# Kernel optimization log

Measured on AMD Instinct MI355X. Metric: run time of the kernel, lower is better.

Reference implementation:

```python
import jax, jax.numpy as jnp
import numpy as np

B, IN, HID, LAT, EH = 32768, 512, 2048, 128, 512
MID = max(HID // 2, LAT * 2)      # 1024
HALF = max(EH // 2, 4)            # 256
EPS = 1e-5
LN10 = float(np.log(10.0))


def setup_inputs() -> dict:
    key = jax.random.key(0)
    ks = jax.random.split(key, 24)
    r = lambda k, shp, s=0.02: (jax.random.normal(k, shp, dtype=jnp.float32) * s)
    d = {
        "x": jax.random.normal(ks[0], (B, IN), dtype=jnp.float32),
        "group_idx": jax.random.randint(ks[1], (B,), 0, 3),
        # encoder: Linear(IN,HID)+BN+ELU, Linear(HID,MID)+BN+ELU, Linear(MID,LAT)
        "e_w1": r(ks[2], (HID, IN)), "e_b1": jnp.zeros((HID,), jnp.float32),
        "e_g1": jnp.ones((HID,), jnp.float32), "e_be1": jnp.zeros((HID,), jnp.float32),
        "e_w2": r(ks[3], (MID, HID)), "e_b2": jnp.zeros((MID,), jnp.float32),
        "e_g2": jnp.ones((MID,), jnp.float32), "e_be2": jnp.zeros((MID,), jnp.float32),
        "e_w3": r(ks[4], (LAT, MID)), "e_b3": jnp.zeros((LAT,), jnp.float32),
        # shared: Linear(LAT+IN,HID)+BN+ELU, Linear(HID,MID)+BN+ELU
        "s_w1": r(ks[5], (HID, LAT + IN)), "s_b1": jnp.zeros((HID,), jnp.float32),
        "s_g1": jnp.ones((HID,), jnp.float32), "s_be1": jnp.zeros((HID,), jnp.float32),
        "s_w2": r(ks[6], (MID, HID)), "s_b2": jnp.zeros((MID,), jnp.float32),
        "s_g2": jnp.ones((MID,), jnp.float32), "s_be2": jnp.zeros((MID,), jnp.float32),
        # 3 expert heads, stacked on leading axis E=3
        "h_w1": r(ks[7], (3, EH, MID)), "h_b1": jnp.zeros((3, EH), jnp.float32),
        "h_w2": r(ks[8], (3, HALF, EH)), "h_b2": jnp.zeros((3, HALF), jnp.float32),
        "h_w3": r(ks[9], (3, HALF)), "h_b3": jnp.zeros((3,), jnp.float32),
    }
    return d


def _bn(h, g, b):
    # BatchNorm1d in training mode: batch mean, biased batch var
    m = jnp.mean(h, axis=0)
    v = jnp.var(h, axis=0)
    return (h - m) * (g / jnp.sqrt(v + EPS)) + b


def _elu(h):
    return jax.nn.elu(h)


def reference(x, group_idx,
              e_w1, e_b1, e_g1, e_be1, e_w2, e_b2, e_g2, e_be2, e_w3, e_b3,
              s_w1, s_b1, s_g1, s_be1, s_w2, s_b2, s_g2, s_be2,
              h_w1, h_b1, h_w2, h_b2, h_w3, h_b3):
    # encoder
    h = _elu(_bn(x @ e_w1.T + e_b1, e_g1, e_be1))
    h = _elu(_bn(h @ e_w2.T + e_b2, e_g2, e_be2))
    latent = h @ e_w3.T + e_b3                              # [B, LAT]
    # shared trunk
    z = jnp.concatenate([latent, x], axis=-1)               # [B, LAT+IN]
    h = _elu(_bn(z @ s_w1.T + s_b1, s_g1, s_be1))
    hidden = _elu(_bn(h @ s_w2.T + s_b2, s_g2, s_be2))      # [B, MID]
    # expert heads: compute all 3 (tiny vs trunk), then select per-row group
    t1 = _elu(jnp.einsum('bm,ehm->ebh', hidden, h_w1) + h_b1[:, None, :])   # [3,B,EH]
    t2 = _elu(jnp.einsum('ebh,efh->ebf', t1, h_w2) + h_b2[:, None, :])      # [3,B,HALF]
    pred_all = jnp.einsum('ebf,ef->eb', t2, h_w3) + h_b3[:, None]           # [3,B]
    pred_raw = jnp.take_along_axis(pred_all, group_idx[None, :], axis=0)[0] # [B]
    pred_log = -jax.nn.softplus(pred_raw)
    pred_prob = jnp.exp(pred_log * jnp.float32(LN10))       # 10 ** pred_log
    return pred_log, pred_prob
```

## Files before the change

### kernel.cpp

```cpp
#include <hip/hip_runtime.h>
#include <math.h>

#define B_    32768
#define LN10_ 2.302585092994046f
#define MT_H  264
#define NBLK  128

typedef __attribute__((ext_vector_type(8))) short short8;
typedef __attribute__((ext_vector_type(4))) float f32x4;

typedef const __attribute__((address_space(1))) void gvoid_t;
typedef __attribute__((address_space(3))) void svoid_t;

__device__ __forceinline__ void gl16(const void* g, void* l) {
  __builtin_amdgcn_global_load_lds((gvoid_t*)g, (svoid_t*)l, 16, 0, 0);
}

__device__ __forceinline__ float bf2f(unsigned int u) {
  union { unsigned int i; float f; } v; v.i = u << 16; return v.f;
}
__device__ __forceinline__ unsigned short f2bf(float f) {
  union { float f; unsigned int i; } v; v.f = f;
  unsigned int x = v.i;
  unsigned int r = x + 0x7FFFu + ((x >> 16) & 1u);
  return (unsigned short)(r >> 16);
}

__global__ __launch_bounds__(512)
void gemm256(const unsigned short* __restrict__ A0_, int lda,
             const unsigned short* __restrict__ W0_, int ldw,
             unsigned short* __restrict__ C0, int ldc, int K,
             float* __restrict__ st, int Ntot) {
  __shared__ __align__(16) unsigned short lds[65536];
  const int t = threadIdx.x;
  const int nx = gridDim.x, ny = gridDim.y;
  const int f = blockIdx.y * nx + blockIdx.x;
  const int xcd = f & 7, g = f >> 3;
  const int gdiv = g / nx;
  const int mt = xcd * (ny >> 3) + gdiv;
  const int nt = g - gdiv * nx;
  const int mBase = mt * 256, nBase = nt * 256;
  const unsigned short* Ap = A0_ + (size_t)mBase * lda;
  const unsigned short* Wp = W0_ + (size_t)nBase * ldw;
  const int w = t >> 6, l = t & 63;
  const int wr = w >> 2, wc = w & 3;
  const int lm = l & 15, lg = l >> 4;

  const int rr = t >> 3;
  const int xc = ((t & 7) ^ (rr & 7)) << 3;
  const unsigned short* gA = Ap + (size_t)rr * lda + xc;
  const unsigned short* gB = Wp + (size_t)rr * ldw + xc;

#define SG(ptr, ld, rowoff, dst) \
    gl16((ptr) + (size_t)(rowoff) * (ld) + ko_, &lds[(dst) + t * 8])
#define STAGE_Aa(tt) { const int d_=((tt)&1)<<15; const size_t ko_=(size_t)(tt)*64; \
    SG(gA,lda,0,d_);          SG(gA,lda,128,d_+8192); }
#define STAGE_Ab(tt) { const int d_=((tt)&1)<<15; const size_t ko_=(size_t)(tt)*64; \
    SG(gA,lda,64,d_+4096);    SG(gA,lda,192,d_+12288); }
#define STAGE_B0(tt) { const int d_=((tt)&1)<<15; const size_t ko_=(size_t)(tt)*64; \
    SG(gB,ldw,0,d_+16384);    SG(gB,ldw,64,d_+20480); }
#define STAGE_B1(tt) { const int d_=((tt)&1)<<15; const size_t ko_=(size_t)(tt)*64; \
    SG(gB,ldw,128,d_+24576);  SG(gB,ldw,192,d_+28672); }

  const int cs0 = ((lg) ^ (l & 7)) << 3;
  const int cs1 = ((4 | lg) ^ (l & 7)) << 3;

  f32x4 acc[8][4];
#pragma unroll
  for (int i = 0; i < 8; ++i)
#pragma unroll
    for (int j = 0; j < 4; ++j) {
      f32x4 z4 = {0.f, 0.f, 0.f, 0.f};
      acc[i][j] = z4;
    }

  const int NT = K >> 6;
  STAGE_Aa(0); STAGE_B0(0); STAGE_B1(0); STAGE_Ab(0);
  if (NT > 1) {
    STAGE_Aa(1); STAGE_B0(1); STAGE_B1(1);
    asm volatile("s_waitcnt vmcnt(6)" ::: "memory");
  } else {
    asm volatile("s_waitcnt vmcnt(0)" ::: "memory");
  }
  __builtin_amdgcn_s_barrier();
  __builtin_amdgcn_sched_barrier(0);

  short8 af[4][2], b01[2][2], b23[2][2];
  for (int tt = 0; tt < NT; ++tt) {
    const int d = (tt & 1) << 15;
    const int abase = d + (wr * 128 + lm) * 64;
    const int bbase = d + 16384 + (wc * 32 + lm) * 64;
    const bool s1ok = (tt + 1 < NT), s2ok = (tt + 2 < NT);
#pragma unroll
    for (int fi = 0; fi < 4; ++fi) {
      af[fi][0] = *(const short8*)&lds[abase + fi * 1024 + cs0];
      af[fi][1] = *(const short8*)&lds[abase + fi * 1024 + cs1];
    }
#pragma unroll
    for (int fj = 0; fj < 2; ++fj) {
      b01[fj][0] = *(const short8*)&lds[bbase + fj * 1024 + cs0];
      b01[fj][1] = *(const short8*)&lds[bbase + fj * 1024 + cs1];
    }
    if (s1ok) STAGE_Ab(tt + 1);
    __builtin_amdgcn_s_barrier();
    asm volatile("s_waitcnt lgkmcnt(0)" ::: "memory");
    __builtin_amdgcn_sched_barrier(0);
    __builtin_amdgcn_s_setprio(1);
#pragma unroll
    for (int fi = 0; fi < 4; ++fi) {
      acc[fi][0] = __builtin_amdgcn_mfma_f32_16x16x32_bf16(af[fi][0], b01[0][0], acc[fi][0], 0, 0, 0);
      acc[fi][0] = __builtin_amdgcn_mfma_f32_16x16x32_bf16(af[fi][1], b01[0][1], acc[fi][0], 0, 0, 0);
      acc[fi][1] = __builtin_amdgcn_mfma_f32_16x16x32_bf16(af[fi][0], b01[1][0], acc[fi][1], 0, 0, 0);
      acc[fi][1] = __builtin_amdgcn_mfma_f32_16x16x32_bf16(af[fi][1], b01[1][1], acc[fi][1], 0, 0, 0);
    }
    __builtin_amdgcn_s_setprio(0);
#pragma unroll
    for (int fj = 0; fj < 2; ++fj) {
      b23[fj][0] = *(const short8*)&lds[bbase + 8192 + fj * 1024 + cs0];
      b23[fj][1] = *(const short8*)&lds[bbase + 8192 + fj * 1024 + cs1];
    }
    if (s2ok) STAGE_Aa(tt + 2);
    __builtin_amdgcn_s_barrier();
    asm volatile("s_waitcnt lgkmcnt(0)" ::: "memory");
    __builtin_amdgcn_sched_barrier(0);
    __builtin_amdgcn_s_setprio(1);
#pragma unroll
    for (int fi = 0; fi < 4; ++fi) {
      acc[fi][2] = __builtin_amdgcn_mfma_f32_16x16x32_bf16(af[fi][0], b23[0][0], acc[fi][2], 0, 0, 0);
      acc[fi][2] = __builtin_amdgcn_mfma_f32_16x16x32_bf16(af[fi][1], b23[0][1], acc[fi][2], 0, 0, 0);
      acc[fi][3] = __builtin_amdgcn_mfma_f32_16x16x32_bf16(af[fi][0], b23[1][0], acc[fi][3], 0, 0, 0);
      acc[fi][3] = __builtin_amdgcn_mfma_f32_16x16x32_bf16(af[fi][1], b23[1][1], acc[fi][3], 0, 0, 0);
    }
    __builtin_amdgcn_s_setprio(0);
#pragma unroll
    for (int fi = 0; fi < 4; ++fi) {
      af[fi][0] = *(const short8*)&lds[abase + 4096 + fi * 1024 + cs0];
      af[fi][1] = *(const short8*)&lds[abase + 4096 + fi * 1024 + cs1];
    }
    if (s2ok) STAGE_B0(tt + 2);
    __builtin_amdgcn_s_barrier();
    asm volatile("s_waitcnt lgkmcnt(0)" ::: "memory");
    __builtin_amdgcn_sched_barrier(0);
    __builtin_amdgcn_s_setprio(1);
#pragma unroll
    for (int fi = 0; fi < 4; ++fi) {
      acc[4 + fi][0] = __builtin_amdgcn_mfma_f32_16x16x32_bf16(af[fi][0], b01[0][0], acc[4 + fi][0], 0, 0, 0);
      acc[4 + fi][0] = __builtin_amdgcn_mfma_f32_16x16x32_bf16(af[fi][1], b01[0][1], acc[4 + fi][0], 0, 0, 0);
      acc[4 + fi][1] = __builtin_amdgcn_mfma_f32_16x16x32_bf16(af[fi][0], b01[1][0], acc[4 + fi][1], 0, 0, 0);
      acc[4 + fi][1] = __builtin_amdgcn_mfma_f32_16x16x32_bf16(af[fi][1], b01[1][1], acc[4 + fi][1], 0, 0, 0);
    }
    __builtin_amdgcn_s_setprio(0);
    if (s2ok) STAGE_B1(tt + 2);
    __builtin_amdgcn_s_setprio(1);
#pragma unroll
    for (int fi = 0; fi < 4; ++fi) {
      acc[4 + fi][2] = __builtin_amdgcn_mfma_f32_16x16x32_bf16(af[fi][0], b23[0][0], acc[4 + fi][2], 0, 0, 0);
      acc[4 + fi][2] = __builtin_amdgcn_mfma_f32_16x16x32_bf16(af[fi][1], b23[0][1], acc[4 + fi][2], 0, 0, 0);
      acc[4 + fi][3] = __builtin_amdgcn_mfma_f32_16x16x32_bf16(af[fi][0], b23[1][0], acc[4 + fi][3], 0, 0, 0);
      acc[4 + fi][3] = __builtin_amdgcn_mfma_f32_16x16x32_bf16(af[fi][1], b23[1][1], acc[4 + fi][3], 0, 0, 0);
    }
    __builtin_amdgcn_s_setprio(0);
    if (s1ok) {
      if (s2ok) { asm volatile("s_waitcnt vmcnt(6)" ::: "memory"); }
      else      { asm volatile("s_waitcnt vmcnt(0)" ::: "memory"); }
      __builtin_amdgcn_s_barrier();
      __builtin_amdgcn_sched_barrier(0);
    }
  }

#pragma unroll
  for (int j = 0; j < 4; ++j) {
    int n = nBase + (j >> 1) * 128 + wc * 32 + (j & 1) * 16 + lm;
    float s1 = 0.f, q1 = 0.f;
#pragma unroll
    for (int i = 0; i < 8; ++i) {
      int m0 = mBase + wr * 128 + i * 16 + lg * 4;
#pragma unroll
      for (int r = 0; r < 4; ++r) {
        float v = acc[i][j][r];
        s1 += v; q1 += v * v;
        C0[(size_t)(m0 + r) * ldc + n] = f2bf(v);
      }
    }
    s1 += __shfl_xor(s1, 16, 64); s1 += __shfl_xor(s1, 32, 64);
    q1 += __shfl_xor(q1, 16, 64); q1 += __shfl_xor(q1, 32, 64);
    if (lg == 0) { atomicAdd(&st[n], s1); atomicAdd(&st[Ntot + n], q1); }
  }
}
#undef SG
#undef STAGE_Aa
#undef STAGE_Ab
#undef STAGE_B0
#undef STAGE_B1

__global__ __launch_bounds__(256)
void gemm_bt(const unsigned short* __restrict__ A0, int lda,
             const unsigned short* __restrict__ W0, int ldw,
             unsigned short* __restrict__ C0, int ldc,
             int K, const float* __restrict__ bias0, int elu,
             float* __restrict__ st, int Ntot,
             long eA, long eW, long eC, int eBias,
             const int* __restrict__ texp) {
  __shared__ __align__(16) unsigned short lA[128 * 64];
  __shared__ __align__(16) unsigned short lB[128 * 64];
  const int t = threadIdx.x;
  const int nx = gridDim.x, ny = gridDim.y;
  const int f = blockIdx.y * nx + blockIdx.x;
  const int xcd = f & 7, g = f >> 3;
  const int gdiv = g / nx;
  const int mt = xcd * (ny >> 3) + gdiv;
  const int nt = g - gdiv * nx;
  const int mBase = mt * 128;
  const int nBase = nt * 128;
  int e = texp ? texp[mt] : (int)blockIdx.z;
  if (e < 0) return;
  const unsigned short* A = A0 + (size_t)e * eA;
  const unsigned short* W = W0 + (size_t)e * eW;
  unsigned short* C = C0 + (size_t)e * eC;
  const float* bias = bias0 ? (bias0 + (size_t)e * eBias) : nullptr;
  const unsigned short* Ap = A + (size_t)mBase * lda;
  const unsigned short* Wp = W + (size_t)nBase * ldw;
  const int w = t >> 6, l = t & 63;
  const int wr = (w >> 1) * 64, wc = (w & 1) * 64;
  const int lm = l & 15, lg = l >> 4;

  f32x4 acc[4][4];
#pragma unroll
  for (int i = 0; i < 4; ++i)
#pragma unroll
    for (int j = 0; j < 4; ++j) {
      f32x4 z4 = {0.f, 0.f, 0.f, 0.f};
      acc[i][j] = z4;
    }

  for (int k0 = 0; k0 < K; k0 += 64) {
    __syncthreads();
#pragma unroll
    for (int it = 0; it < 4; ++it) {
      int chunk = it * 256 + t;
      int row = chunk >> 3, sc = chunk & 7;
      int gc = (sc ^ (row & 7)) << 3;
      gl16(Ap + (size_t)row * lda + k0 + gc, &lA[chunk * 8]);
      gl16(Wp + (size_t)row * ldw + k0 + gc, &lB[chunk * 8]);
    }
    __syncthreads();
#pragma unroll
    for (int kk = 0; kk < 64; kk += 32) {
      short8 af[4], bfr[4];
#pragma unroll
      for (int i = 0; i < 4; ++i) {
        int ar = wr + i * 16 + lm;
        int ac = (kk >> 3) + lg;
        af[i] = *(const short8*)&lA[ar * 64 + ((ac ^ (ar & 7)) << 3)];
      }
#pragma unroll
      for (int j = 0; j < 4; ++j) {
        int br = wc + j * 16 + lm;
        int bc = (kk >> 3) + lg;
        bfr[j] = *(const short8*)&lB[br * 64 + ((bc ^ (br & 7)) << 3)];
      }
#pragma unroll
      for (int i = 0; i < 4; ++i)
#pragma unroll
        for (int j = 0; j < 4; ++j)
          acc[i][j] = __builtin_amdgcn_mfma_f32_16x16x32_bf16(af[i], bfr[j], acc[i][j], 0, 0, 0);
    }
  }

#pragma unroll
  for (int j = 0; j < 4; ++j) {
    int n = nBase + wc + j * 16 + lm;
    float bj = bias ? bias[n] : 0.f;
    float s = 0.f, q = 0.f;
#pragma unroll
    for (int i = 0; i < 4; ++i) {
      int m0 = mBase + wr + i * 16 + lg * 4;
#pragma unroll
      for (int r = 0; r < 4; ++r) {
        float v = acc[i][j][r] + bj;
        if (elu) v = v > 0.f ? v : expm1f(v);
        s += v; q += v * v;
        C[(size_t)(m0 + r) * ldc + n] = f2bf(v);
      }
    }
    if (st) {
      s += __shfl_xor(s, 16, 64); s += __shfl_xor(s, 32, 64);
      q += __shfl_xor(q, 16, 64); q += __shfl_xor(q, 32, 64);
      if (lg == 0) { atomicAdd(&st[n], s); atomicAdd(&st[Ntot + n], q); }
    }
  }
}

__global__ void bn_apply(unsigned short* __restrict__ Y, const float* __restrict__ st,
                         const float* __restrict__ gam, const float* __restrict__ bet,
                         int N, float invB) {
  size_t i = (size_t)blockIdx.x * blockDim.x + threadIdx.x;
  size_t base = i * 8;
  int col = (int)(base & (size_t)(N - 1));
  float a8[8], b8[8];
#pragma unroll
  for (int k = 0; k < 8; ++k) {
    int c = col + k;
    float m = st[c] * invB;
    float var = st[N + c] * invB - m * m;
    float av = gam[c] * rsqrtf(var + 1e-5f);
    a8[k] = av;
    b8[k] = bet[c] - m * av;
  }
  uint4 u = *(uint4*)&Y[base];
  unsigned int uu[4] = {u.x, u.y, u.z, u.w};
  unsigned int oo[4];
#pragma unroll
  for (int k = 0; k < 4; ++k) {
    float vlo = bf2f(uu[k] & 0xFFFFu);
    float vhi = bf2f(uu[k] >> 16);
    float flo = a8[2 * k] * vlo + b8[2 * k];
    float fhi = a8[2 * k + 1] * vhi + b8[2 * k + 1];
    flo = flo > 0.f ? flo : expm1f(flo);
    fhi = fhi > 0.f ? fhi : expm1f(fhi);
    oo[k] = (unsigned int)f2bf(flo) | ((unsigned int)f2bf(fhi) << 16);
  }
  uint4 o = {oo[0], oo[1], oo[2], oo[3]};
  *(uint4*)&Y[base] = o;
}

__global__ void cast_all(const float* __restrict__ e1, const float* __restrict__ e2,
                         const float* __restrict__ e3, const float* __restrict__ s1,
                         const float* __restrict__ s2, const float* __restrict__ h1,
                         const float* __restrict__ h2, unsigned short* __restrict__ dst) {
  int i4 = blockIdx.x * 256 + threadIdx.x;
  const float* src;
  int rel;
  if (i4 < 786432) {
    if (i4 < 262144) { src = e1; rel = i4; }
    else             { src = e2; rel = i4 - 262144; }
  } else if (i4 < 1146880) {
    if (i4 < 819200) { src = e3; rel = i4 - 786432; }
    else             { src = s1; rel = i4 - 819200; }
  } else if (i4 < 2064384) {
    if (i4 < 1671168) { src = s2; rel = i4 - 1146880; }
    else              { src = h1; rel = i4 - 1671168; }
  } else { src = h2; rel = i4 - 2064384; }
  float4 v = ((const float4*)src)[rel];
  ushort4 o = {f2bf(v.x), f2bf(v.y), f2bf(v.z), f2bf(v.w)};
  ((ushort4*)dst)[i4] = o;
}

__global__ void cast_x(const float* __restrict__ x, unsigned short* __restrict__ z) {
  int i = blockIdx.x * blockDim.x + threadIdx.x;
  int b = i >> 7;
  int c = (i & 127) << 2;
  float4 v = *(const float4*)&x[(size_t)b * 512 + c];
  ushort4 o = {f2bf(v.x), f2bf(v.y), f2bf(v.z), f2bf(v.w)};
  *(ushort4*)&z[(size_t)b * 640 + 128 + c] = o;
}

__global__ void hist_blocks(const int* __restrict__ gidx, int* __restrict__ bcnt) {
  int blk = blockIdx.x;
  int i = blk * 256 + threadIdx.x;
  int e = gidx[i];
  int l = threadIdx.x & 63, w = threadIdx.x >> 6;
  __shared__ int wc[4][3];
  unsigned long long m0 = __ballot(e == 0);
  unsigned long long m1 = __ballot(e == 1);
  unsigned long long m2 = __ballot(e == 2);
  if (l == 0) { wc[w][0] = __popcll(m0); wc[w][1] = __popcll(m1); wc[w][2] = __popcll(m2); }
  __syncthreads();
  if (threadIdx.x < 3)
    bcnt[blk * 3 + threadIdx.x] = wc[0][threadIdx.x] + wc[1][threadIdx.x] +
                                  wc[2][threadIdx.x] + wc[3][threadIdx.x];
}

__global__ void scan_plan(const int* __restrict__ bcnt, int* __restrict__ boff,
                          int* __restrict__ vend, int* __restrict__ texp) {
  __shared__ int sp[4];
  __shared__ int cnt[3];
  int t = threadIdx.x;
  if (t < 3) {
    int s = 0;
    for (int b = 0; b < NBLK; ++b) s += bcnt[b * 3 + t];
    cnt[t] = s;
  }
  __syncthreads();
  if (t == 0) {
    int p = 0;
    for (int e = 0; e < 3; ++e) {
      sp[e] = p; vend[e] = p + cnt[e];
      p += ((cnt[e] + 127) >> 7) << 7;
    }
    sp[3] = p;
  }
  __syncthreads();
  if (t < 3) {
    int run = sp[t];
    for (int b = 0; b < NBLK; ++b) { boff[b * 3 + t] = run; run += bcnt[b * 3 + t]; }
  }
  if (t < MT_H) {
    int r0 = t << 7, e = -1;
    for (int k = 0; k < 3; ++k)
      if (r0 >= sp[k] && r0 < sp[k + 1]) e = k;
    texp[t] = e;
  }
}

__global__ void scatter2(const int* __restrict__ gidx, const int* __restrict__ boff,
                         int* __restrict__ perm) {
  int blk = blockIdx.x;
  int i = blk * 256 + threadIdx.x;
  int e = gidx[i];
  int l = threadIdx.x & 63, w = threadIdx.x >> 6;
  __shared__ int wc[4][3];
  unsigned long long m0 = __ballot(e == 0);
  unsigned long long m1 = __ballot(e == 1);
  unsigned long long m2 = __ballot(e == 2);
  if (l == 0) { wc[w][0] = __popcll(m0); wc[w][1] = __popcll(m1); wc[w][2] = __popcll(m2); }
  __syncthreads();
  unsigned long long me = (e == 0) ? m0 : ((e == 1) ? m1 : m2);
  int rank = __popcll(me & ((1ull << l) - 1ull));
  int woff = 0;
  for (int ww = 0; ww < w; ++ww) woff += wc[ww][e];
  perm[boff[blk * 3 + e] + woff + rank] = i;
}

__global__ void gather_bn(const unsigned short* __restrict__ hid, const int* __restrict__ perm,
                          const int* __restrict__ texp, const int* __restrict__ vend,
                          const float* __restrict__ st, const float* __restrict__ gam,
                          const float* __restrict__ bet, float invB,
                          unsigned short* __restrict__ ht) {
  int idx = blockIdx.x * 256 + threadIdx.x;
  int p = idx >> 7, c8 = (idx & 127) << 3;
  int e = texp[p >> 7];
  uint4 o = {0u, 0u, 0u, 0u};
  if (e >= 0 && p < vend[e]) {
    float a8[8], b8[8];
#pragma unroll
    for (int k = 0; k < 8; ++k) {
      int c = c8 + k;
      float m = st[c] * invB;
      float var = st[1024 + c] * invB - m * m;
      float av = gam[c] * rsqrtf(var + 1e-5f);
      a8[k] = av;
      b8[k] = bet[c] - m * av;
    }
    int src = perm[p];
    uint4 u = *(const uint4*)&hid[(size_t)src * 1024 + c8];
    unsigned int uu[4] = {u.x, u.y, u.z, u.w};
    unsigned int oo[4];
#pragma unroll
    for (int k = 0; k < 4; ++k) {
      float vlo = bf2f(uu[k] & 0xFFFFu);
      float vhi = bf2f(uu[k] >> 16);
      float flo = a8[2 * k] * vlo + b8[2 * k];
      float fhi = a8[2 * k + 1] * vhi + b8[2 * k + 1];
      flo = flo > 0.f ? flo : expm1f(flo);
      fhi = fhi > 0.f ? fhi : expm1f(fhi);
      oo[k] = (unsigned int)f2bf(flo) | ((unsigned int)f2bf(fhi) << 16);
    }
    o.x = oo[0]; o.y = oo[1]; o.z = oo[2]; o.w = oo[3];
  }
  *(uint4*)&ht[(size_t)p * 1024 + c8] = o;
}

__global__ void final_pred(const unsigned short* __restrict__ t2, const int* __restrict__ perm,
                           const int* __restrict__ texp, const int* __restrict__ vend,
                           const float* __restrict__ w3, const float* __restrict__ b3,
                           float* __restrict__ out) {
  int p = blockIdx.x * 4 + (threadIdx.x >> 6);
  int l = threadIdx.x & 63;
  int e = texp[p >> 7];
  if (e < 0 || p >= vend[e]) return;
  ushort4 u = *(const ushort4*)&t2[(size_t)p * 256 + l * 4];
  float4 wv = *(const float4*)&w3[e * 256 + l * 4];
  float sum = bf2f(u.x) * wv.x + bf2f(u.y) * wv.y + bf2f(u.z) * wv.z + bf2f(u.w) * wv.w;
#pragma unroll
  for (int off = 32; off; off >>= 1) sum += __shfl_down(sum, off, 64);
  if (l == 0) {
    int orig = perm[p];
    float xr = sum + b3[e];
    float sp = (xr > 0.f) ? (xr + log1pf(expf(-xr))) : log1pf(expf(xr));
    float pl = -sp;
    out[orig] = pl;
    out[B_ + orig] = expf(pl * LN10_);
  }
}

extern "C" void kernel_launch(void* const* d_in, const int* in_sizes, int n_in,
                              void* d_out, int out_size, void* d_ws, size_t ws_size,
                              hipStream_t stream) {
  const float* x    = (const float*)d_in[0];
  const int*   gidx = (const int*)d_in[1];
  const float* e_w1 = (const float*)d_in[2];
  const float* e_g1 = (const float*)d_in[4];
  const float* e_be1= (const float*)d_in[5];
  const float* e_w2 = (const float*)d_in[6];
  const float* e_g2 = (const float*)d_in[8];
  const float* e_be2= (const float*)d_in[9];
  const float* e_w3 = (const float*)d_in[10];
  const float* e_b3 = (const float*)d_in[11];
  const float* s_w1 = (const float*)d_in[12];
  const float* s_g1 = (const float*)d_in[14];
  const float* s_be1= (const float*)d_in[15];
  const float* s_w2 = (const float*)d_in[16];
  const float* s_g2 = (const float*)d_in[18];
  const float* s_be2= (const float*)d_in[19];
  const float* h_w1 = (const float*)d_in[20];
  const float* h_b1 = (const float*)d_in[21];
  const float* h_w2 = (const float*)d_in[22];
  const float* h_b2 = (const float*)d_in[23];
  const float* h_w3 = (const float*)d_in[24];
  const float* h_b3 = (const float*)d_in[25];
  float* out = (float*)d_out;

  char* ws = (char*)d_ws;
  size_t off = 0;
  auto alloc = [&](size_t bytes) -> char* {
    char* p = ws + off;
    off += (bytes + 255) & ~(size_t)255;
    return p;
  };
  unsigned short* wb_e1 = (unsigned short*)alloc((size_t)2048 * 512 * 2);
  unsigned short* wb_e2 = (unsigned short*)alloc((size_t)1024 * 2048 * 2);
  unsigned short* wb_e3 = (unsigned short*)alloc((size_t)128 * 1024 * 2);
  unsigned short* wb_s1 = (unsigned short*)alloc((size_t)2048 * 640 * 2);
  unsigned short* wb_s2 = (unsigned short*)alloc((size_t)1024 * 2048 * 2);
  unsigned short* wb_h1 = (unsigned short*)alloc((size_t)3 * 512 * 1024 * 2);
  unsigned short* wb_h2 = (unsigned short*)alloc((size_t)3 * 256 * 512 * 2);
  unsigned short* z     = (unsigned short*)alloc((size_t)B_ * 640 * 2);
  unsigned short* bufA  = (unsigned short*)alloc((size_t)B_ * 2048 * 2);
  unsigned short* bufB  = (unsigned short*)alloc((size_t)B_ * 1024 * 2);
  float* st = (float*)alloc(12288 * sizeof(float));
  float* st0 = st;
  float* st1 = st + 4096;
  float* st2 = st + 6144;
  float* st3 = st + 10240;
  int* bcnt = (int*)alloc(NBLK * 3 * sizeof(int));
  int* boff = (int*)alloc(NBLK * 3 * sizeof(int));
  int* vend = (int*)alloc(3 * sizeof(int));
  int* texp = (int*)alloc(MT_H * sizeof(int));
  int* perm = (int*)alloc((size_t)MT_H * 128 * sizeof(int));
  unsigned short* ht  = bufA;
  unsigned short* t1p = bufA + (size_t)MT_H * 128 * 1024;
  unsigned short* t2p = z;

  cast_all<<<8448, 256, 0, stream>>>(e_w1, e_w2, e_w3, s_w1, s_w2, h_w1, h_w2, wb_e1);
  cast_x<<<(B_ * 128) / 256, 256, 0, stream>>>(x, z);
  hipMemsetAsync(st, 0, 12288 * sizeof(float), stream);
  hist_blocks<<<NBLK, 256, 0, stream>>>(gidx, bcnt);
  scan_plan<<<1, 512, 0, stream>>>(bcnt, boff, vend, texp);
  scatter2<<<NBLK, 256, 0, stream>>>(gidx, boff, perm);

  gemm256<<<dim3(8, 128), 512, 0, stream>>>(z + 128, 640, wb_e1, 512, bufA, 2048, 512,
                                            st0, 2048);
  bn_apply<<<B_, 256, 0, stream>>>(bufA, st0, e_g1, e_be1, 2048, 1.0f / B_);
  gemm256<<<dim3(4, 128), 512, 0, stream>>>(bufA, 2048, wb_e2, 2048, bufB, 1024, 2048,
                                            st1, 1024);
  bn_apply<<<B_ / 2, 256, 0, stream>>>(bufB, st1, e_g2, e_be2, 1024, 1.0f / B_);
  gemm_bt<<<dim3(1, 256), 256, 0, stream>>>(bufB, 1024, wb_e3, 1024, z, 640, 1024,
                                            e_b3, 0, nullptr, 0, 0, 0, 0, 0, nullptr);
  gemm256<<<dim3(8, 128), 512, 0, stream>>>(z, 640, wb_s1, 640, bufA, 2048, 640,
                                            st2, 2048);
  bn_apply<<<B_, 256, 0, stream>>>(bufA, st2, s_g1, s_be1, 2048, 1.0f / B_);
  gemm256<<<dim3(4, 128), 512, 0, stream>>>(bufA, 2048, wb_s2, 2048, bufB, 1024, 2048,
                                            st3, 1024);

  gather_bn<<<(MT_H * 128 * 128) / 256, 256, 0, stream>>>(bufB, perm, texp, vend,
                                                          st3, s_g2, s_be2, 1.0f / B_, ht);

  gemm_bt<<<dim3(4, MT_H), 256, 0, stream>>>(ht, 1024, wb_h1, 1024, t1p, 512, 1024,
                                             h_b1, 1, nullptr, 0,
                                             0, (long)512 * 1024, 0, 512, texp);
  gemm_bt<<<dim3(2, MT_H), 256, 0, stream>>>(t1p, 512, wb_h2, 512, t2p, 256, 512,
                                             h_b2, 1, nullptr, 0,
                                             0, (long)256 * 512, 0, 256, texp);

  final_pred<<<(MT_H * 128) / 4, 256, 0, stream>>>(t2p, perm, texp, vend, h_w3, h_b3, out);
}
```

Before: 940.1 us.

## Fuse BN+ELU and row gather into the A-operand load of small GEMMs

The standalone BN-apply pass before the encoder's latent GEMM and the gather_bn kernel before the first expert-head GEMM are removed. A new gemm_btf kernel loads A rows through registers, optionally via a permutation index, and applies precomputed per-column BN scale/shift plus ELU before writing to LDS. A tiny bn_coef kernel precomputes those coefficients. This saves full read/write passes over the B×1024 activation, but it replaces async global_load_lds with register-staged loads and recomputes the transform once per N-tile (4 times for the first head GEMM).

```diff
diff --git a/kernel.cpp b/kernel.cpp
--- a/kernel.cpp
+++ b/kernel.cpp
@@ -194,13 +194,14 @@
 #undef STAGE_B1
 
 __global__ __launch_bounds__(256)
-void gemm_bt(const unsigned short* __restrict__ A0, int lda,
-             const unsigned short* __restrict__ W0, int ldw,
-             unsigned short* __restrict__ C0, int ldc,
-             int K, const float* __restrict__ bias0, int elu,
-             float* __restrict__ st, int Ntot,
-             long eA, long eW, long eC, int eBias,
-             const int* __restrict__ texp) {
+void gemm_btf(const unsigned short* __restrict__ A0, int lda,
+              const unsigned short* __restrict__ W0, int ldw,
+              unsigned short* __restrict__ C0, int ldc,
+              int K, const float* __restrict__ bias0, int elu,
+              long eW, int eBias,
+              const int* __restrict__ texp,
+              const int* __restrict__ perm, const int* __restrict__ vend,
+              const float* __restrict__ coef) {
   __shared__ __align__(16) unsigned short lA[128 * 64];
   __shared__ __align__(16) unsigned short lB[128 * 64];
   const int t = threadIdx.x;
@@ -212,18 +213,32 @@
   const int nt = g - gdiv * nx;
   const int mBase = mt * 128;
   const int nBase = nt * 128;
-  int e = texp ? texp[mt] : (int)blockIdx.z;
+  int e = texp ? texp[mt] : 0;
   if (e < 0) return;
-  const unsigned short* A = A0 + (size_t)e * eA;
-  const unsigned short* W = W0 + (size_t)e * eW;
-  unsigned short* C = C0 + (size_t)e * eC;
+  const unsigned short* Wp = W0 + (size_t)e * eW + (size_t)nBase * ldw;
   const float* bias = bias0 ? (bias0 + (size_t)e * eBias) : nullptr;
-  const unsigned short* Ap = A + (size_t)mBase * lda;
-  const unsigned short* Wp = W + (size_t)nBase * ldw;
   const int w = t >> 6, l = t & 63;
   const int wr = (w >> 1) * 64, wc = (w & 1) * 64;
   const int lm = l & 15, lg = l >> 4;
 
+  const int sc = t & 7;
+  int aRow[4], aCol[4];
+  bool aVld[4];
+#pragma unroll
+  for (int it = 0; it < 4; ++it) {
+    int r = it * 32 + (t >> 3);
+    aCol[it] = (sc ^ (r & 7)) << 3;
+    int gr = mBase + r;
+    if (perm) {
+      bool v = gr < vend[e];
+      aVld[it] = v;
+      aRow[it] = v ? perm[gr] : 0;
+    } else {
+      aVld[it] = true;
+      aRow[it] = gr;
+    }
+  }
+
   f32x4 acc[4][4];
 #pragma unroll
   for (int i = 0; i < 4; ++i)
@@ -238,10 +253,40 @@
 #pragma unroll
     for (int it = 0; it < 4; ++it) {
       int chunk = it * 256 + t;
-      int row = chunk >> 3, sc = chunk & 7;
+      int row = chunk >> 3;
       int gc = (sc ^ (row & 7)) << 3;
-      gl16(Ap + (size_t)row * lda + k0 + gc, &lA[chunk * 8]);
       gl16(Wp + (size_t)row * ldw + k0 + gc, &lB[chunk * 8]);
+    }
+#pragma unroll
+    for (int it = 0; it < 4; ++it) {
+      int chunk = it * 256 + t;
+      uint4 v = {0u, 0u, 0u, 0u};
+      if (aVld[it]) {
+        v = *(const uint4*)&A0[(size_t)aRow[it] * lda + k0 + aCol[it]];
+        if (coef) {
+          int c = k0 + aCol[it];
+          float4 a0 = *(const float4*)&coef[c];
+          float4 a1 = *(const float4*)&coef[c + 4];
+          float4 b0 = *(const float4*)&coef[K + c];
+          float4 b1 = *(const float4*)&coef[K + c + 4];
+          float a8[8] = {a0.x, a0.y, a0.z, a0.w, a1.x, a1.y, a1.z, a1.w};
+          float b8[8] = {b0.x, b0.y, b0.z, b0.w, b1.x, b1.y, b1.z, b1.w};
+          unsigned int uu[4] = {v.x, v.y, v.z, v.w};
+          unsigned int oo[4];
+#pragma unroll
+          for (int k2 = 0; k2 < 4; ++k2) {
+            float vlo = bf2f(uu[k2] & 0xFFFFu);
+            float vhi = bf2f(uu[k2] >> 16);
+            float flo = a8[2 * k2] * vlo + b8[2 * k2];
+            float fhi = a8[2 * k2 + 1] * vhi + b8[2 * k2 + 1];
+            flo = flo > 0.f ? flo : expm1f(flo);
+            fhi = fhi > 0.f ? fhi : expm1f(fhi);
+            oo[k2] = (unsigned int)f2bf(flo) | ((unsigned int)f2bf(fhi) << 16);
+          }
+          v.x = oo[0]; v.y = oo[1]; v.z = oo[2]; v.w = oo[3];
+        }
+      }
+      *(uint4*)&lA[chunk * 8] = v;
     }
     __syncthreads();
 #pragma unroll
@@ -271,7 +316,6 @@
   for (int j = 0; j < 4; ++j) {
     int n = nBase + wc + j * 16 + lm;
     float bj = bias ? bias[n] : 0.f;
-    float s = 0.f, q = 0.f;
 #pragma unroll
     for (int i = 0; i < 4; ++i) {
       int m0 = mBase + wr + i * 16 + lg * 4;
@@ -279,16 +323,21 @@
       for (int r = 0; r < 4; ++r) {
         float v = acc[i][j][r] + bj;
         if (elu) v = v > 0.f ? v : expm1f(v);
-        s += v; q += v * v;
-        C[(size_t)(m0 + r) * ldc + n] = f2bf(v);
+        C0[(size_t)(m0 + r) * ldc + n] = f2bf(v);
       }
     }
-    if (st) {
-      s += __shfl_xor(s, 16, 64); s += __shfl_xor(s, 32, 64);
-      q += __shfl_xor(q, 16, 64); q += __shfl_xor(q, 32, 64);
-      if (lg == 0) { atomicAdd(&st[n], s); atomicAdd(&st[Ntot + n], q); }
-    }
-  }
+  }
+}
+
+__global__ void bn_coef(const float* __restrict__ st, const float* __restrict__ gam,
+                        const float* __restrict__ bet, float* __restrict__ coef,
+                        int N, float invB) {
+  int c = blockIdx.x * 256 + threadIdx.x;
+  float m = st[c] * invB;
+  float var = st[N + c] * invB - m * m;
+  float av = gam[c] * rsqrtf(var + 1e-5f);
+  coef[c] = av;
+  coef[N + c] = bet[c] - m * av;
 }
 
 __global__ void bn_apply(unsigned short* __restrict__ Y, const float* __restrict__ st,
@@ -420,45 +469,6 @@
   int woff = 0;
   for (int ww = 0; ww < w; ++ww) woff += wc[ww][e];
   perm[boff[blk * 3 + e] + woff + rank] = i;
-}
-
-__global__ void gather_bn(const unsigned short* __restrict__ hid, const int* __restrict__ perm,
-                          const int* __restrict__ texp, const int* __restrict__ vend,
-                          const float* __restrict__ st, const float* __restrict__ gam,
-                          const float* __restrict__ bet, float invB,
-                          unsigned short* __restrict__ ht) {
-  int idx = blockIdx.x * 256 + threadIdx.x;
-  int p = idx >> 7, c8 = (idx & 127) << 3;
-  int e = texp[p >> 7];
-  uint4 o = {0u, 0u, 0u, 0u};
-  if (e >= 0 && p < vend[e]) {
-    float a8[8], b8[8];
-#pragma unroll
-    for (int k = 0; k < 8; ++k) {
-      int c = c8 + k;
-      float m = st[c] * invB;
-      float var = st[1024 + c] * invB - m * m;
-      float av = gam[c] * rsqrtf(var + 1e-5f);
-      a8[k] = av;
-      b8[k] = bet[c] - m * av;
-    }
-    int src = perm[p];
-    uint4 u = *(const uint4*)&hid[(size_t)src * 1024 + c8];
-    unsigned int uu[4] = {u.x, u.y, u.z, u.w};
-    unsigned int oo[4];
-#pragma unroll
-    for (int k = 0; k < 4; ++k) {
-      float vlo = bf2f(uu[k] & 0xFFFFu);
-      float vhi = bf2f(uu[k] >> 16);
-      float flo = a8[2 * k] * vlo + b8[2 * k];
-      float fhi = a8[2 * k + 1] * vhi + b8[2 * k + 1];
-      flo = flo > 0.f ? flo : expm1f(flo);
-      fhi = fhi > 0.f ? fhi : expm1f(fhi);
-      oo[k] = (unsigned int)f2bf(flo) | ((unsigned int)f2bf(fhi) << 16);
-    }
-    o.x = oo[0]; o.y = oo[1]; o.z = oo[2]; o.w = oo[3];
-  }
-  *(uint4*)&ht[(size_t)p * 1024 + c8] = o;
 }
 
 __global__ void final_pred(const unsigned short* __restrict__ t2, const int* __restrict__ perm,
@@ -533,12 +543,13 @@
   float* st1 = st + 4096;
   float* st2 = st + 6144;
   float* st3 = st + 10240;
+  float* coefA = (float*)alloc(2048 * sizeof(float));
+  float* coefB = (float*)alloc(2048 * sizeof(float));
   int* bcnt = (int*)alloc(NBLK * 3 * sizeof(int));
   int* boff = (int*)alloc(NBLK * 3 * sizeof(int));
   int* vend = (int*)alloc(3 * sizeof(int));
   int* texp = (int*)alloc(MT_H * sizeof(int));
   int* perm = (int*)alloc((size_t)MT_H * 128 * sizeof(int));
-  unsigned short* ht  = bufA;
   unsigned short* t1p = bufA + (size_t)MT_H * 128 * 1024;
   unsigned short* t2p = z;
 
@@ -554,24 +565,23 @@
   bn_apply<<<B_, 256, 0, stream>>>(bufA, st0, e_g1, e_be1, 2048, 1.0f / B_);
   gemm256<<<dim3(4, 128), 512, 0, stream>>>(bufA, 2048, wb_e2, 2048, bufB, 1024, 2048,
                                             st1, 1024);
-  bn_apply<<<B_ / 2, 256, 0, stream>>>(bufB, st1, e_g2, e_be2, 1024, 1.0f / B_);
-  gemm_bt<<<dim3(1, 256), 256, 0, stream>>>(bufB, 1024, wb_e3, 1024, z, 640, 1024,
-                                            e_b3, 0, nullptr, 0, 0, 0, 0, 0, nullptr);
+  bn_coef<<<4, 256, 0, stream>>>(st1, e_g2, e_be2, coefA, 1024, 1.0f / B_);
+  gemm_btf<<<dim3(1, 256), 256, 0, stream>>>(bufB, 1024, wb_e3, 1024, z, 640, 1024,
+                                             e_b3, 0, 0, 0,
+                                             nullptr, nullptr, nullptr, coefA);
   gemm256<<<dim3(8, 128), 512, 0, stream>>>(z, 640, wb_s1, 640, bufA, 2048, 640,
                                             st2, 2048);
   bn_apply<<<B_, 256, 0, stream>>>(bufA, st2, s_g1, s_be1, 2048, 1.0f / B_);
   gemm256<<<dim3(4, 128), 512, 0, stream>>>(bufA, 2048, wb_s2, 2048, bufB, 1024, 2048,
                                             st3, 1024);
-
-  gather_bn<<<(MT_H * 128 * 128) / 256, 256, 0, stream>>>(bufB, perm, texp, vend,
-                                                          st3, s_g2, s_be2, 1.0f / B_, ht);
-
-  gemm_bt<<<dim3(4, MT_H), 256, 0, stream>>>(ht, 1024, wb_h1, 1024, t1p, 512, 1024,
-                                             h_b1, 1, nullptr, 0,
-                                             0, (long)512 * 1024, 0, 512, texp);
-  gemm_bt<<<dim3(2, MT_H), 256, 0, stream>>>(t1p, 512, wb_h2, 512, t2p, 256, 512,
-                                             h_b2, 1, nullptr, 0,
-                                             0, (long)256 * 512, 0, 256, texp);
+  bn_coef<<<4, 256, 0, stream>>>(st3, s_g2, s_be2, coefB, 1024, 1.0f / B_);
+
+  gemm_btf<<<dim3(4, MT_H), 256, 0, stream>>>(bufB, 1024, wb_h1, 1024, t1p, 512, 1024,
+                                              h_b1, 1, (long)512 * 1024, 512,
+                                              texp, perm, vend, coefB);
+  gemm_btf<<<dim3(2, MT_H), 256, 0, stream>>>(t1p, 512, wb_h2, 512, t2p, 256, 512,
+                                              h_b2, 1, (long)256 * 512, 256,
+                                              texp, nullptr, nullptr, nullptr);
 
   final_pred<<<(MT_H * 128) / 4, 256, 0, stream>>>(t2p, perm, texp, vend, h_w3, h_b3, out);
 }
```

Measured after the change: 1.035 ms. 10.1% more time.
